# Kernel tuning notes

Measured on AMD Instinct MI355X. Metric: run time of the kernel, lower is better.

Reference implementation:

```python
import jax, jax.numpy as jnp
import numpy as np

H_IMG, W_IMG = 32, 32   # image_size -> seq_len = 1024
NH, HD, D = 8, 32, 256  # num_heads, head_dim, d_model
B = 8


def _relative_positions(h, w):
    # Swin-style relative position index table, [h*w, h*w] int32
    y = np.arange(h); x = np.arange(w)
    coords = np.stack(np.meshgrid(y, x, indexing='ij')).reshape(2, -1)  # [2, S]
    rel = coords[:, :, None] - coords[:, None, :]                      # [2, S, S]
    rel = rel.transpose(1, 2, 0).astype(np.int64)                      # [S, S, 2]
    rel[:, :, 0] += h - 1
    rel[:, :, 1] += w - 1
    rel[:, :, 0] *= 2 * w - 1
    return np.int32(rel.sum(-1))                                       # [S, S]

_POS = _relative_positions(H_IMG, W_IMG)


def setup_inputs() -> dict:
    key = jax.random.key(0)
    ks = jax.random.split(key, 8)
    S = H_IMG * W_IMG
    return {
        'inputs_q': jax.random.normal(ks[0], (B, S, D), jnp.float32),
        'inputs_kv': jax.random.normal(ks[1], (B, S, D), jnp.float32),
        'Wq': jax.random.normal(ks[2], (D, NH, HD), jnp.float32) / np.sqrt(D),
        'bq': jnp.zeros((NH, HD), jnp.float32),
        'Wk': jax.random.normal(ks[3], (D, NH, HD), jnp.float32) / np.sqrt(D),
        'bk': jnp.zeros((NH, HD), jnp.float32),
        'Wv': jax.random.normal(ks[4], (D, NH, HD), jnp.float32) / np.sqrt(D),
        'bv': jnp.zeros((NH, HD), jnp.float32),
        'rel_table': 0.02 * jax.random.normal(ks[5], ((2 * H_IMG - 1) * (2 * W_IMG - 1), NH), jnp.float32),
        'Wo': jax.random.normal(ks[6], (NH, HD, D), jnp.float32) / np.sqrt(NH * HD),
        'bo': jnp.zeros((D,), jnp.float32),
    }


def reference(inputs_q, inputs_kv, Wq, bq, Wk, bk, Wv, bv, rel_table, Wo, bo):
    pos = jnp.asarray(_POS)                                  # [S, S] int32 (constant)
    q = jnp.einsum('bsd,dhk->bshk', inputs_q, Wq) + bq       # [B, S, H, HD]
    k = jnp.einsum('bsd,dhk->bshk', inputs_kv, Wk) + bk
    v = jnp.einsum('bsd,dhk->bshk', inputs_kv, Wv) + bv
    q = q / jnp.sqrt(jnp.asarray(HD, q.dtype))
    attn = jnp.einsum('bqhd,bkhd->bhqk', q, k)               # [B, H, S, S]
    rel_bias = rel_table[pos]                                # [S, S, H]
    attn = attn + jnp.transpose(rel_bias, (2, 0, 1))[None]   # broadcast over batch
    attn = jax.nn.softmax(attn, axis=-1)
    x = jnp.einsum('bhqk,bkhd->bqhd', attn, v)               # [B, S, H, HD]
    return jnp.einsum('bqhd,hdf->bqf', x, Wo) + bo           # [B, S, D]
```

## Files before the change

### kernel.cpp

```cpp
#include <hip/hip_runtime.h>

#define B_SZ   8
#define S_LEN  1024
#define D_MOD  256
#define NHEADS 8
#define LOG2E  1.4426950408889634f
#define QSCALE_LOG2E 0.2550352766751165f

typedef _Float16 f16x8 __attribute__((ext_vector_type(8)));
typedef _Float16 f16x4 __attribute__((ext_vector_type(4)));
typedef float    f32x4 __attribute__((ext_vector_type(4)));

__global__ __launch_bounds__(256)
void prep_kernel(const float* __restrict__ Wq, const float* __restrict__ Wk,
                 const float* __restrict__ Wv, const float* __restrict__ Wo,
                 const float* __restrict__ rel,
                 _Float16* __restrict__ wtp, _Float16* __restrict__ tabh) {
    if (blockIdx.x < 32) {
        __shared__ _Float16 Wl[32 * 264];
        const int mi = blockIdx.x >> 3;
        const int k0 = (blockIdx.x & 7) << 5;
        const float* W = (mi == 0) ? Wq : (mi == 1) ? Wk : (mi == 2) ? Wv : Wo;
        {
            const int r  = threadIdx.x >> 3;
            const int c4 = (threadIdx.x & 7) * 4;
            const float* src = W + (size_t)(k0 + r) * 256 + c4;
#pragma unroll
            for (int g = 0; g < 8; ++g) {
                f32x4 v = *(const f32x4*)(src + g * 32);
                f16x4 o;
#pragma unroll
                for (int j = 0; j < 4; ++j) o[j] = (_Float16)v[j];
                *(f16x4*)(&Wl[r * 264 + c4 + g * 32]) = o;
            }
        }
        __syncthreads();
        const int n16 = threadIdx.x >> 4;
        const int l16 = threadIdx.x & 15;
        const int kk  = k0 >> 5;
#pragma unroll
        for (int quad = 0; quad < 4; ++quad) {
            f16x8 v;
#pragma unroll
            for (int j = 0; j < 8; ++j) v[j] = Wl[(quad * 8 + j) * 264 + n16 * 16 + l16];
            *(f16x8*)(wtp + (((size_t)(mi * 16 + n16) * 8 + kk) << 9) + (quad * 16 + l16) * 8) = v;
        }
        return;
    }
    __shared__ float rl[63 * 8];
    const int dy31 = blockIdx.x - 32;
    for (int f = threadIdx.x; f < 504; f += 256) rl[f] = rel[(size_t)dy31 * 504 + f];
    __syncthreads();
    const int h  = threadIdx.x >> 5;
    const int r5 = threadIdx.x & 31;
#pragma unroll
    for (int c = 0; c < 6; ++c) {
        const int oi   = r5 * 6 + c;
        const int e    = oi >> 6;
        const int lane = oi & 63;
        const int quad = lane >> 4, l16 = lane & 15;
        f16x4 v;
#pragma unroll
        for (int reg = 0; reg < 4; ++reg) {
            const int idx = 16 * e + l16 - quad * 4 - reg + 15;
            v[reg] = (_Float16)(rl[idx * 8 + h] * LOG2E);
        }
        *(f16x4*)(tabh + (((size_t)(h * 63 + dy31) * 3 + e) << 8) + lane * 4) = v;
    }
}

__global__ __launch_bounds__(256)
void gemm_qkv_kernel(const float* __restrict__ in_q, const float* __restrict__ in_kv,
                     const _Float16* __restrict__ wtp,
                     const float* __restrict__ bq, const float* __restrict__ bk,
                     const float* __restrict__ bv,
                     _Float16* __restrict__ qs, _Float16* __restrict__ ks,
                     _Float16* __restrict__ vs) {
    __shared__ __align__(16) _Float16 Lds[256 * 40];
    const int tid  = threadIdx.x;
    const int w    = tid >> 6;
    const int lane = tid & 63;
    const int quad = lane >> 4;
    const int l16  = lane & 15;
    const int mt = blockIdx.x;
    const int z  = blockIdx.y;
    const int m0 = mt * 32;
    const int b  = mt >> 5, t = mt & 31;

    {
        const int r  = tid >> 3;
        const int c4 = (tid & 7) * 4;
        const float* src = (z ? in_kv : in_q) + (size_t)(m0 + r) * 256 + c4;
        _Float16* dst = Lds + r * 264 + c4;
#pragma unroll
        for (int g = 0; g < 8; ++g) {
            f32x4 v = *(const f32x4*)(src + g * 32);
            f16x4 o;
#pragma unroll
            for (int j = 0; j < 4; ++j) o[j] = (_Float16)v[j];
            *(f16x4*)(dst + g * 32) = o;
        }
    }
    __syncthreads();

    f32x4 acc[2][4];
#pragma unroll
    for (int jj = 0; jj < 2; ++jj)
#pragma unroll
        for (int i = 0; i < 4; ++i) acc[jj][i] = (f32x4){0.f, 0.f, 0.f, 0.f};

#pragma unroll
    for (int kk = 0; kk < 8; ++kk) {
        const int k8 = kk * 32 + quad * 8;
        f16x8 a0 = *(const f16x8*)(Lds + l16 * 264 + k8);
        f16x8 a1 = *(const f16x8*)(Lds + (16 + l16) * 264 + k8);
#pragma unroll
        for (int i = 0; i < 4; ++i) {
            f16x8 wv = *(const f16x8*)(wtp + (((size_t)(z * 16 + w * 4 + i) * 8 + kk) << 9) + lane * 8);
            if (z < 2) {
                acc[0][i] = __builtin_amdgcn_mfma_f32_16x16x32_f16(wv, a0, acc[0][i], 0, 0, 0);
                acc[1][i] = __builtin_amdgcn_mfma_f32_16x16x32_f16(wv, a1, acc[1][i], 0, 0, 0);
            } else {
                acc[0][i] = __builtin_amdgcn_mfma_f32_16x16x32_f16(a0, wv, acc[0][i], 0, 0, 0);
                acc[1][i] = __builtin_amdgcn_mfma_f32_16x16x32_f16(a1, wv, acc[1][i], 0, 0, 0);
            }
        }
    }
    __syncthreads();

    if (z < 2) {
        const float* bias = z ? bk : bq;
        const float  sc   = z ? 1.0f : QSCALE_LOG2E;
#pragma unroll
        for (int i = 0; i < 4; ++i) {
            f32x4 b4 = *(const f32x4*)(bias + (w * 4 + i) * 16 + quad * 4);
#pragma unroll
            for (int jj = 0; jj < 2; ++jj) {
                f16x4 pk;
#pragma unroll
                for (int r = 0; r < 4; ++r) pk[r] = (_Float16)((acc[jj][i][r] + b4[r]) * sc);
                *(f16x4*)(Lds + (jj * 16 + l16) * 264 + (w * 4 + i) * 16 + quad * 4) = pk;
            }
        }
        __syncthreads();
        _Float16* dst = z ? ks : qs;
#pragma unroll
        for (int c = 0; c < 4; ++c) {
            const int sg = w * 4 + c;
            const int sub = sg >> 3, h = sg & 7;
            f16x8 v = *(const f16x8*)(Lds + (sub * 16 + l16) * 264 + h * 32 + quad * 8);
            *(f16x8*)(dst + (((size_t)((b * 8 + h) * 32 + t) * 2 + sub) << 9) + lane * 8) = v;
        }
    } else {
#pragma unroll
        for (int i = 0; i < 4; ++i) {
            const float bvv = bv[(w * 4 + i) * 16 + l16];
#pragma unroll
            for (int jj = 0; jj < 2; ++jj) {
                f16x4 pk;
#pragma unroll
                for (int r = 0; r < 4; ++r) pk[r] = (_Float16)(acc[jj][i][r] + bvv);
                *(f16x4*)(Lds + ((w * 4 + i) * 16 + l16) * 40 + jj * 16 + quad * 4) = pk;
            }
        }
        __syncthreads();
#pragma unroll
        for (int c = 0; c < 4; ++c) {
            const int sg = w * 4 + c;
            const int sub = sg >> 3, h = sg & 7;
            f16x8 v = *(const f16x8*)(Lds + (h * 32 + sub * 16 + l16) * 40 + quad * 8);
            *(f16x8*)(vs + (((size_t)((b * 8 + h) * 32 + t) * 2 + sub) << 9) + lane * 8) = v;
        }
    }
}

__global__ __launch_bounds__(256)
void gemm_out_kernel(const _Float16* __restrict__ xs, const _Float16* __restrict__ wtp,
                     const float* __restrict__ bo, float* __restrict__ out) {
    const int tid  = threadIdx.x;
    const int w    = tid >> 6;
    const int lane = tid & 63;
    const int quad = lane >> 4;
    const int l16  = lane & 15;
    const int bx = blockIdx.x, by = blockIdx.y;
    const int mt0  = bx * 4 + (w & 1) * 2;
    const int n16a = by * 4 + (w >> 1) * 2;

    f32x4 acc[2][2];
#pragma unroll
    for (int i = 0; i < 2; ++i)
#pragma unroll
        for (int j = 0; j < 2; ++j) acc[i][j] = (f32x4){0.f, 0.f, 0.f, 0.f};

#pragma unroll
    for (int kk = 0; kk < 8; ++kk) {
        f16x8 a0 = *(const f16x8*)(xs + (((size_t)(mt0 + 0) * 8 + kk) << 9) + lane * 8);
        f16x8 a1 = *(const f16x8*)(xs + (((size_t)(mt0 + 1) * 8 + kk) << 9) + lane * 8);
        f16x8 b0 = *(const f16x8*)(wtp + (((size_t)(48 + n16a + 0) * 8 + kk) << 9) + lane * 8);
        f16x8 b1 = *(const f16x8*)(wtp + (((size_t)(48 + n16a + 1) * 8 + kk) << 9) + lane * 8);
        acc[0][0] = __builtin_amdgcn_mfma_f32_16x16x32_f16(a0, b0, acc[0][0], 0, 0, 0);
        acc[0][1] = __builtin_amdgcn_mfma_f32_16x16x32_f16(a0, b1, acc[0][1], 0, 0, 0);
        acc[1][0] = __builtin_amdgcn_mfma_f32_16x16x32_f16(a1, b0, acc[1][0], 0, 0, 0);
        acc[1][1] = __builtin_amdgcn_mfma_f32_16x16x32_f16(a1, b1, acc[1][1], 0, 0, 0);
    }

#pragma unroll
    for (int i = 0; i < 2; ++i) {
        const int col = (n16a + i) * 16 + l16;
        const float bvv = bo[col];
#pragma unroll
        for (int jj = 0; jj < 2; ++jj) {
#pragma unroll
            for (int r = 0; r < 4; ++r) {
                const int row = (mt0 + jj) * 16 + quad * 4 + r;
                out[(size_t)row * 256 + col] = acc[jj][i][r] + bvv;
            }
        }
    }
}

__global__ __launch_bounds__(256)
void attn_kernel(const _Float16* __restrict__ qs, const _Float16* __restrict__ ks,
                 const _Float16* __restrict__ vs, const _Float16* __restrict__ tabh,
                 _Float16* __restrict__ xs) {
    __shared__ __align__(16) _Float16 Ps[4][32][40];

    const int tid  = threadIdx.x;
    const int w    = tid >> 6;
    const int lane = tid & 63;
    const int quad = lane >> 4;
    const int l16  = lane & 15;

    const int n     = blockIdx.x;
    const int xcd   = n & 7;
    const int local = n >> 3;
    const int bh    = xcd * 8 + (local & 7);
    const int qc    = local >> 3;
    const int b = bh >> 3, h = bh & 7;
    const int qrow_base = qc * 128 + w * 32;
    const int yq = qc * 4 + w;

    const _Float16* qp = qs + (((size_t)(bh * 32 + yq) * 2) << 9) + lane * 8;
    const f16x8 qf0 = *(const f16x8*)(qp);
    const f16x8 qf1 = *(const f16x8*)(qp + 512);
    const _Float16* kp = ks + (((size_t)bh * 64) << 9) + lane * 8;
    const _Float16* vp = vs + (((size_t)bh * 64) << 9) + lane * 8;
    const _Float16* tb = tabh + (((size_t)h * 189) << 8) + lane * 4;

    f16x8 ones;
#pragma unroll
    for (int j = 0; j < 8; ++j) ones[j] = (_Float16)1.0f;

    f32x4 o00 = {0.f,0.f,0.f,0.f}, o01 = {0.f,0.f,0.f,0.f};
    f32x4 o10 = {0.f,0.f,0.f,0.f}, o11 = {0.f,0.f,0.f,0.f};
    f32x4 ol0 = {0.f,0.f,0.f,0.f}, ol1 = {0.f,0.f,0.f,0.f};

    f16x8 kf0 = *(const f16x8*)(kp);
    f16x8 kf1 = *(const f16x8*)(kp + 512);
    f16x8 vf0 = *(const f16x8*)(vp);
    f16x8 vf1 = *(const f16x8*)(vp + 512);
    f32x4 c0, c1, c2;
    {
        f16x4 t0 = *(const f16x4*)(tb + (((yq + 31) * 3 + 0) << 8));
        f16x4 t1 = *(const f16x4*)(tb + (((yq + 31) * 3 + 1) << 8));
        f16x4 t2 = *(const f16x4*)(tb + (((yq + 31) * 3 + 2) << 8));
#pragma unroll
        for (int r = 0; r < 4; ++r) {
            c0[r] = (float)t0[r]; c1[r] = (float)t1[r]; c2[r] = (float)t2[r];
        }
    }

    for (int kt = 0; kt < 32; ++kt) {
        const bool more = (kt < 31);
        f16x8 nk0, nk1, nv0, nv1;
        f16x4 nt0, nt1, nt2;
        if (more) {
            const _Float16* kq = kp + (kt + 1) * 1024;
            nk0 = *(const f16x8*)(kq);
            nk1 = *(const f16x8*)(kq + 512);
            const _Float16* vq = vp + (kt + 1) * 1024;
            nv0 = *(const f16x8*)(vq);
            nv1 = *(const f16x8*)(vq + 512);
            const int d = (yq + 30 - kt) * 3;
            nt0 = *(const f16x4*)(tb + ((d + 0) << 8));
            nt1 = *(const f16x4*)(tb + ((d + 1) << 8));
            nt2 = *(const f16x4*)(tb + ((d + 2) << 8));
        }

        f32x4 s00 = __builtin_amdgcn_mfma_f32_16x16x32_f16(kf0, qf0, c1, 0, 0, 0);
        f32x4 s01 = __builtin_amdgcn_mfma_f32_16x16x32_f16(kf1, qf0, c0, 0, 0, 0);
        f32x4 s10 = __builtin_amdgcn_mfma_f32_16x16x32_f16(kf0, qf1, c2, 0, 0, 0);
        f32x4 s11 = __builtin_amdgcn_mfma_f32_16x16x32_f16(kf1, qf1, c1, 0, 0, 0);

        f16x4 p;
#pragma unroll
        for (int r = 0; r < 4; ++r) p[r] = (_Float16)__builtin_amdgcn_exp2f(s00[r]);
        *(f16x4*)(&Ps[w][l16][quad * 4]) = p;
#pragma unroll
        for (int r = 0; r < 4; ++r) p[r] = (_Float16)__builtin_amdgcn_exp2f(s01[r]);
        *(f16x4*)(&Ps[w][l16][16 + quad * 4]) = p;
#pragma unroll
        for (int r = 0; r < 4; ++r) p[r] = (_Float16)__builtin_amdgcn_exp2f(s10[r]);
        *(f16x4*)(&Ps[w][16 + l16][quad * 4]) = p;
#pragma unroll
        for (int r = 0; r < 4; ++r) p[r] = (_Float16)__builtin_amdgcn_exp2f(s11[r]);
        *(f16x4*)(&Ps[w][16 + l16][16 + quad * 4]) = p;

        const f16x8 pf0 = *(const f16x8*)(&Ps[w][l16][quad * 8]);
        const f16x8 pf1 = *(const f16x8*)(&Ps[w][16 + l16][quad * 8]);
        o00 = __builtin_amdgcn_mfma_f32_16x16x32_f16(vf0, pf0, o00, 0, 0, 0);
        o01 = __builtin_amdgcn_mfma_f32_16x16x32_f16(vf0, pf1, o01, 0, 0, 0);
        o10 = __builtin_amdgcn_mfma_f32_16x16x32_f16(vf1, pf0, o10, 0, 0, 0);
        o11 = __builtin_amdgcn_mfma_f32_16x16x32_f16(vf1, pf1, o11, 0, 0, 0);
        ol0 = __builtin_amdgcn_mfma_f32_16x16x32_f16(ones, pf0, ol0, 0, 0, 0);
        ol1 = __builtin_amdgcn_mfma_f32_16x16x32_f16(ones, pf1, ol1, 0, 0, 0);

        if (more) {
            kf0 = nk0; kf1 = nk1; vf0 = nv0; vf1 = nv1;
#pragma unroll
            for (int r = 0; r < 4; ++r) {
                c0[r] = (float)nt0[r]; c1[r] = (float)nt1[r]; c2[r] = (float)nt2[r];
            }
        }
    }

#pragma unroll
    for (int qsub = 0; qsub < 2; ++qsub) {
        const f32x4 olo = qsub ? o01 : o00;
        const f32x4 ohi = qsub ? o11 : o10;
        const f32x4 ll  = qsub ? ol1 : ol0;
        const float inv = __builtin_amdgcn_rcpf(ll[0]);
        f16x4 u, v;
#pragma unroll
        for (int r = 0; r < 4; ++r) {
            u[r] = (_Float16)(olo[r] * inv);
            v[r] = (_Float16)(ohi[r] * inv);
        }
        *(f16x4*)(&Ps[w][qsub * 16 + l16][quad * 4]) = u;
        *(f16x4*)(&Ps[w][qsub * 16 + l16][16 + quad * 4]) = v;
    }
#pragma unroll
    for (int qsub = 0; qsub < 2; ++qsub) {
        f16x8 af = *(const f16x8*)(&Ps[w][qsub * 16 + l16][quad * 8]);
        const int mtile = b * 64 + qc * 8 + w * 2 + qsub;
        *(f16x8*)(xs + (((size_t)mtile * 8 + h) << 9) + lane * 8) = af;
    }
}

extern "C" void kernel_launch(void* const* d_in, const int* in_sizes, int n_in,
                              void* d_out, int out_size, void* d_ws, size_t ws_size,
                              hipStream_t stream) {
    const float* in_q  = (const float*)d_in[0];
    const float* in_kv = (const float*)d_in[1];
    const float* Wq    = (const float*)d_in[2];
    const float* bq    = (const float*)d_in[3];
    const float* Wk    = (const float*)d_in[4];
    const float* bk    = (const float*)d_in[5];
    const float* Wv    = (const float*)d_in[6];
    const float* bv    = (const float*)d_in[7];
    const float* rel   = (const float*)d_in[8];
    const float* Wo    = (const float*)d_in[9];
    const float* bo    = (const float*)d_in[10];
    float* out = (float*)d_out;

    char* wsb = (char*)d_ws;
    _Float16* qs   = (_Float16*)(wsb);
    _Float16* ks   = (_Float16*)(wsb + (size_t)4  * 1048576);
    _Float16* vs   = (_Float16*)(wsb + (size_t)8  * 1048576);
    _Float16* xs   = (_Float16*)(wsb + (size_t)12 * 1048576);
    _Float16* wtp  = (_Float16*)(wsb + (size_t)16 * 1048576);
    _Float16* tabh = (_Float16*)(wsb + (size_t)17 * 1048576);

    const dim3 blk(256);

    prep_kernel<<<dim3(95), blk, 0, stream>>>(Wq, Wk, Wv, Wo, rel, wtp, tabh);
    gemm_qkv_kernel<<<dim3(256, 3), blk, 0, stream>>>(
        in_q, in_kv, wtp, bq, bk, bv, qs, ks, vs);
    attn_kernel<<<dim3(512), blk, 0, stream>>>(qs, ks, vs, tabh, xs);
    gemm_out_kernel<<<dim3(128, 4), blk, 0, stream>>>(xs, wtp, bo, out);
}
```

Measured before the change: 127.3 us.

## Halve per-wave query tile in attention and prefetch weights in QKV GEMM

The attention kernel now gives each wave 16 query rows instead of 32 and launches twice as many blocks (1024), which cuts per-wave MFMA work and register pressure in exchange for loading each K/V tile twice as often. Relative-bias table entries are selected by sub-tile parity. Separately, the QKV GEMM software-pipelines its weight and LDS operand loads one k-step ahead, so global load latency overlaps with the MFMAs. The cost is more K/V and table memory traffic across blocks and extra registers in the GEMM.

```diff
diff --git a/kernel.cpp b/kernel.cpp
--- a/kernel.cpp
+++ b/kernel.cpp
@@ -109,21 +109,38 @@
 #pragma unroll
         for (int i = 0; i < 4; ++i) acc[jj][i] = (f32x4){0.f, 0.f, 0.f, 0.f};
 
+    const _Float16* wbase = wtp + (((size_t)(z * 16 + w * 4) * 8) << 9) + lane * 8;
+    f16x8 wc[4], wn[4];
+#pragma unroll
+    for (int i = 0; i < 4; ++i) wc[i] = *(const f16x8*)(wbase + ((i * 8) << 9));
+    f16x8 a0 = *(const f16x8*)(Lds + l16 * 264 + quad * 8);
+    f16x8 a1 = *(const f16x8*)(Lds + (16 + l16) * 264 + quad * 8);
+
 #pragma unroll
     for (int kk = 0; kk < 8; ++kk) {
-        const int k8 = kk * 32 + quad * 8;
-        f16x8 a0 = *(const f16x8*)(Lds + l16 * 264 + k8);
-        f16x8 a1 = *(const f16x8*)(Lds + (16 + l16) * 264 + k8);
+        f16x8 a0n, a1n;
+        if (kk < 7) {
+#pragma unroll
+            for (int i = 0; i < 4; ++i)
+                wn[i] = *(const f16x8*)(wbase + ((i * 8 + kk + 1) << 9));
+            const int k8 = (kk + 1) * 32 + quad * 8;
+            a0n = *(const f16x8*)(Lds + l16 * 264 + k8);
+            a1n = *(const f16x8*)(Lds + (16 + l16) * 264 + k8);
+        }
 #pragma unroll
         for (int i = 0; i < 4; ++i) {
-            f16x8 wv = *(const f16x8*)(wtp + (((size_t)(z * 16 + w * 4 + i) * 8 + kk) << 9) + lane * 8);
             if (z < 2) {
-                acc[0][i] = __builtin_amdgcn_mfma_f32_16x16x32_f16(wv, a0, acc[0][i], 0, 0, 0);
-                acc[1][i] = __builtin_amdgcn_mfma_f32_16x16x32_f16(wv, a1, acc[1][i], 0, 0, 0);
+                acc[0][i] = __builtin_amdgcn_mfma_f32_16x16x32_f16(wc[i], a0, acc[0][i], 0, 0, 0);
+                acc[1][i] = __builtin_amdgcn_mfma_f32_16x16x32_f16(wc[i], a1, acc[1][i], 0, 0, 0);
             } else {
-                acc[0][i] = __builtin_amdgcn_mfma_f32_16x16x32_f16(a0, wv, acc[0][i], 0, 0, 0);
-                acc[1][i] = __builtin_amdgcn_mfma_f32_16x16x32_f16(a1, wv, acc[1][i], 0, 0, 0);
-            }
+                acc[0][i] = __builtin_amdgcn_mfma_f32_16x16x32_f16(a0, wc[i], acc[0][i], 0, 0, 0);
+                acc[1][i] = __builtin_amdgcn_mfma_f32_16x16x32_f16(a1, wc[i], acc[1][i], 0, 0, 0);
+            }
+        }
+        if (kk < 7) {
+#pragma unroll
+            for (int i = 0; i < 4; ++i) wc[i] = wn[i];
+            a0 = a0n; a1 = a1n;
         }
     }
     __syncthreads();
@@ -223,7 +240,7 @@
 void attn_kernel(const _Float16* __restrict__ qs, const _Float16* __restrict__ ks,
                  const _Float16* __restrict__ vs, const _Float16* __restrict__ tabh,
                  _Float16* __restrict__ xs) {
-    __shared__ __align__(16) _Float16 Ps[4][32][40];
+    __shared__ __align__(16) _Float16 Ps[4][16][40];
 
     const int tid  = threadIdx.x;
     const int w    = tid >> 6;
@@ -237,12 +254,14 @@
     const int bh    = xcd * 8 + (local & 7);
     const int qc    = local >> 3;
     const int b = bh >> 3, h = bh & 7;
-    const int qrow_base = qc * 128 + w * 32;
-    const int yq = qc * 4 + w;
-
-    const _Float16* qp = qs + (((size_t)(bh * 32 + yq) * 2) << 9) + lane * 8;
-    const f16x8 qf0 = *(const f16x8*)(qp);
-    const f16x8 qf1 = *(const f16x8*)(qp + 512);
+    const int qrow_base = qc * 64 + w * 16;
+    const int yq  = qrow_base >> 5;
+    const int sub = (qrow_base >> 4) & 1;
+    const int e0  = sub + 1;
+    const int e1  = sub;
+
+    const f16x8 qf =
+        *(const f16x8*)(qs + (((size_t)(bh * 32 + yq) * 2 + sub) << 9) + lane * 8);
     const _Float16* kp = ks + (((size_t)bh * 64) << 9) + lane * 8;
     const _Float16* vp = vs + (((size_t)bh * 64) << 9) + lane * 8;
     const _Float16* tb = tabh + (((size_t)h * 189) << 8) + lane * 4;
@@ -251,29 +270,24 @@
 #pragma unroll
     for (int j = 0; j < 8; ++j) ones[j] = (_Float16)1.0f;
 
-    f32x4 o00 = {0.f,0.f,0.f,0.f}, o01 = {0.f,0.f,0.f,0.f};
-    f32x4 o10 = {0.f,0.f,0.f,0.f}, o11 = {0.f,0.f,0.f,0.f};
-    f32x4 ol0 = {0.f,0.f,0.f,0.f}, ol1 = {0.f,0.f,0.f,0.f};
+    f32x4 o0 = {0.f,0.f,0.f,0.f}, o1 = {0.f,0.f,0.f,0.f}, ol = {0.f,0.f,0.f,0.f};
 
     f16x8 kf0 = *(const f16x8*)(kp);
     f16x8 kf1 = *(const f16x8*)(kp + 512);
     f16x8 vf0 = *(const f16x8*)(vp);
     f16x8 vf1 = *(const f16x8*)(vp + 512);
-    f32x4 c0, c1, c2;
+    f32x4 c0, c1;
     {
-        f16x4 t0 = *(const f16x4*)(tb + (((yq + 31) * 3 + 0) << 8));
-        f16x4 t1 = *(const f16x4*)(tb + (((yq + 31) * 3 + 1) << 8));
-        f16x4 t2 = *(const f16x4*)(tb + (((yq + 31) * 3 + 2) << 8));
-#pragma unroll
-        for (int r = 0; r < 4; ++r) {
-            c0[r] = (float)t0[r]; c1[r] = (float)t1[r]; c2[r] = (float)t2[r];
-        }
+        f16x4 t0 = *(const f16x4*)(tb + (((yq + 31) * 3 + e0) << 8));
+        f16x4 t1 = *(const f16x4*)(tb + (((yq + 31) * 3 + e1) << 8));
+#pragma unroll
+        for (int r = 0; r < 4; ++r) { c0[r] = (float)t0[r]; c1[r] = (float)t1[r]; }
     }
 
     for (int kt = 0; kt < 32; ++kt) {
         const bool more = (kt < 31);
         f16x8 nk0, nk1, nv0, nv1;
-        f16x4 nt0, nt1, nt2;
+        f16x4 nt0, nt1;
         if (more) {
             const _Float16* kq = kp + (kt + 1) * 1024;
             nk0 = *(const f16x8*)(kq);
@@ -282,69 +296,45 @@
             nv0 = *(const f16x8*)(vq);
             nv1 = *(const f16x8*)(vq + 512);
             const int d = (yq + 30 - kt) * 3;
-            nt0 = *(const f16x4*)(tb + ((d + 0) << 8));
-            nt1 = *(const f16x4*)(tb + ((d + 1) << 8));
-            nt2 = *(const f16x4*)(tb + ((d + 2) << 8));
-        }
-
-        f32x4 s00 = __builtin_amdgcn_mfma_f32_16x16x32_f16(kf0, qf0, c1, 0, 0, 0);
-        f32x4 s01 = __builtin_amdgcn_mfma_f32_16x16x32_f16(kf1, qf0, c0, 0, 0, 0);
-        f32x4 s10 = __builtin_amdgcn_mfma_f32_16x16x32_f16(kf0, qf1, c2, 0, 0, 0);
-        f32x4 s11 = __builtin_amdgcn_mfma_f32_16x16x32_f16(kf1, qf1, c1, 0, 0, 0);
+            nt0 = *(const f16x4*)(tb + ((d + e0) << 8));
+            nt1 = *(const f16x4*)(tb + ((d + e1) << 8));
+        }
+
+        f32x4 s0 = __builtin_amdgcn_mfma_f32_16x16x32_f16(kf0, qf, c0, 0, 0, 0);
+        f32x4 s1 = __builtin_amdgcn_mfma_f32_16x16x32_f16(kf1, qf, c1, 0, 0, 0);
 
         f16x4 p;
 #pragma unroll
-        for (int r = 0; r < 4; ++r) p[r] = (_Float16)__builtin_amdgcn_exp2f(s00[r]);
+        for (int r = 0; r < 4; ++r) p[r] = (_Float16)__builtin_amdgcn_exp2f(s0[r]);
         *(f16x4*)(&Ps[w][l16][quad * 4]) = p;
 #pragma unroll
-        for (int r = 0; r < 4; ++r) p[r] = (_Float16)__builtin_amdgcn_exp2f(s01[r]);
+        for (int r = 0; r < 4; ++r) p[r] = (_Float16)__builtin_amdgcn_exp2f(s1[r]);
         *(f16x4*)(&Ps[w][l16][16 + quad * 4]) = p;
-#pragma unroll
-        for (int r = 0; r < 4; ++r) p[r] = (_Float16)__builtin_amdgcn_exp2f(s10[r]);
-        *(f16x4*)(&Ps[w][16 + l16][quad * 4]) = p;
-#pragma unroll
-        for (int r = 0; r < 4; ++r) p[r] = (_Float16)__builtin_amdgcn_exp2f(s11[r]);
-        *(f16x4*)(&Ps[w][16 + l16][16 + quad * 4]) = p;
-
-        const f16x8 pf0 = *(const f16x8*)(&Ps[w][l16][quad * 8]);
-        const f16x8 pf1 = *(const f16x8*)(&Ps[w][16 + l16][quad * 8]);
-        o00 = __builtin_amdgcn_mfma_f32_16x16x32_f16(vf0, pf0, o00, 0, 0, 0);
-        o01 = __builtin_amdgcn_mfma_f32_16x16x32_f16(vf0, pf1, o01, 0, 0, 0);
-        o10 = __builtin_amdgcn_mfma_f32_16x16x32_f16(vf1, pf0, o10, 0, 0, 0);
-        o11 = __builtin_amdgcn_mfma_f32_16x16x32_f16(vf1, pf1, o11, 0, 0, 0);
-        ol0 = __builtin_amdgcn_mfma_f32_16x16x32_f16(ones, pf0, ol0, 0, 0, 0);
-        ol1 = __builtin_amdgcn_mfma_f32_16x16x32_f16(ones, pf1, ol1, 0, 0, 0);
+
+        const f16x8 pf = *(const f16x8*)(&Ps[w][l16][quad * 8]);
+        o0 = __builtin_amdgcn_mfma_f32_16x16x32_f16(vf0, pf, o0, 0, 0, 0);
+        o1 = __builtin_amdgcn_mfma_f32_16x16x32_f16(vf1, pf, o1, 0, 0, 0);
+        ol = __builtin_amdgcn_mfma_f32_16x16x32_f16(ones, pf, ol, 0, 0, 0);
 
         if (more) {
             kf0 = nk0; kf1 = nk1; vf0 = nv0; vf1 = nv1;
 #pragma unroll
-            for (int r = 0; r < 4; ++r) {
-                c0[r] = (float)nt0[r]; c1[r] = (float)nt1[r]; c2[r] = (float)nt2[r];
-            }
-        }
-    }
-
-#pragma unroll
-    for (int qsub = 0; qsub < 2; ++qsub) {
-        const f32x4 olo = qsub ? o01 : o00;
-        const f32x4 ohi = qsub ? o11 : o10;
-        const f32x4 ll  = qsub ? ol1 : ol0;
-        const float inv = __builtin_amdgcn_rcpf(ll[0]);
-        f16x4 u, v;
-#pragma unroll
-        for (int r = 0; r < 4; ++r) {
-            u[r] = (_Float16)(olo[r] * inv);
-            v[r] = (_Float16)(ohi[r] * inv);
-        }
-        *(f16x4*)(&Ps[w][qsub * 16 + l16][quad * 4]) = u;
-        *(f16x4*)(&Ps[w][qsub * 16 + l16][16 + quad * 4]) = v;
-    }
-#pragma unroll
-    for (int qsub = 0; qsub < 2; ++qsub) {
-        f16x8 af = *(const f16x8*)(&Ps[w][qsub * 16 + l16][quad * 8]);
-        const int mtile = b * 64 + qc * 8 + w * 2 + qsub;
-        *(f16x8*)(xs + (((size_t)mtile * 8 + h) << 9) + lane * 8) = af;
-    }
+            for (int r = 0; r < 4; ++r) { c0[r] = (float)nt0[r]; c1[r] = (float)nt1[r]; }
+        }
+    }
+
+    const float inv = __builtin_amdgcn_rcpf(ol[0]);
+    f16x4 u, v;
+#pragma unroll
+    for (int r = 0; r < 4; ++r) {
+        u[r] = (_Float16)(o0[r] * inv);
+        v[r] = (_Float16)(o1[r] * inv);
+    }
+    *(f16x4*)(&Ps[w][l16][quad * 4]) = u;
+    *(f16x4*)(&Ps[w][l16][16 + quad * 4]) = v;
+    const f16x8 af = *(const f16x8*)(&Ps[w][l16][quad * 8]);
+    const int mtile = b * 64 + qc * 4 + w;
+    *(f16x8*)(xs + (((size_t)mtile * 8 + h) << 9) + lane * 8) = af;
 }
 
 extern "C" void kernel_launch(void* const* d_in, const int* in_sizes, int n_in,
@@ -376,6 +366,6 @@
     prep_kernel<<<dim3(95), blk, 0, stream>>>(Wq, Wk, Wv, Wo, rel, wtp, tabh);
     gemm_qkv_kernel<<<dim3(256, 3), blk, 0, stream>>>(
         in_q, in_kv, wtp, bq, bk, bv, qs, ks, vs);
-    attn_kernel<<<dim3(512), blk, 0, stream>>>(qs, ks, vs, tabh, xs);
+    attn_kernel<<<dim3(1024), blk, 0, stream>>>(qs, ks, vs, tabh, xs);
     gemm_out_kernel<<<dim3(128, 4), blk, 0, stream>>>(xs, wtp, bo, out);
 }
```

Measured after the change: 131.3 us. 3.1% more time.
